# Performance work log

Measured on AMD Instinct MI355X. Metric: run time of the kernel, lower is better.

## Reference

```python
import jax, jax.numpy as jnp
import numpy as np
import math

D_MODEL = 1024
HEADS = 16
HEAD_DIM = D_MODEL // HEADS
BATCH = 2
SEQ = 2048


def setup_inputs() -> dict:
    key = jax.random.key(0)
    ks = jax.random.split(key, 6)
    scale = 1.0 / math.sqrt(D_MODEL)
    return {
        "x": jax.random.normal(ks[0], (BATCH, SEQ, D_MODEL), dtype=jnp.float32),
        "mask": jnp.zeros((SEQ, SEQ), dtype=jnp.float32),
        "w_qkv": jax.random.normal(ks[1], (D_MODEL, 3 * D_MODEL), dtype=jnp.float32) * scale,
        "b_qkv": jax.random.normal(ks[2], (3 * D_MODEL,), dtype=jnp.float32) * 0.01,
        "w_out": jax.random.normal(ks[3], (D_MODEL, D_MODEL), dtype=jnp.float32) * scale,
        "b_out": jax.random.normal(ks[4], (D_MODEL,), dtype=jnp.float32) * 0.01,
    }


def reference(x, mask, w_qkv, b_qkv, w_out, b_out):
    B, S, D = x.shape
    H, hd = HEADS, HEAD_DIM
    # fused QKV projection: [B,S,3D]
    qkv = x @ w_qkv + b_qkv
    # [B,S,H,3*hd] -> [B,H,S,3*hd]
    qkv = qkv.reshape(B, S, H, 3 * hd).transpose(0, 2, 1, 3)
    q, k, v = jnp.split(qkv, 3, axis=-1)  # each [B,H,S,hd]
    inv_sqrt_d = jnp.asarray(1.0 / math.sqrt(hd), dtype=x.dtype)
    scores = jnp.einsum("bhqd,bhkd->bhqk", q, k) * inv_sqrt_d
    # additive mask; [S,S] broadcasts identically in [H,B,S,S] or [B,H,S,S] layout
    scores = scores + mask
    attn = jax.nn.softmax(scores, axis=-1)
    vals = jnp.einsum("bhqk,bhkd->bhqd", attn, v)  # [B,H,S,hd]
    vals = vals.transpose(0, 2, 1, 3).reshape(B, S, H * hd)
    return vals @ w_out + b_out
```

## Files before the change

kernel.cpp:

```cpp
#include <hip/hip_runtime.h>


typedef __bf16 bf16;
typedef __bf16 bf16x2 __attribute__((ext_vector_type(2)));
typedef __bf16 bf16x4 __attribute__((ext_vector_type(4)));
typedef __bf16 bf16x8 __attribute__((ext_vector_type(8)));
typedef float f32x4 __attribute__((ext_vector_type(4)));

#define MFMA(a, b, c) __builtin_amdgcn_mfma_f32_16x16x32_bf16((a), (b), (c), 0, 0, 0)

#if __has_builtin(__builtin_amdgcn_exp2f)
#define EXP2(x) __builtin_amdgcn_exp2f(x)
#else
#define EXP2(x) exp2f(x)
#endif

__device__ __forceinline__ void load_lds16(const bf16* g, void* l) {
    __builtin_amdgcn_global_load_lds(
        (const __attribute__((address_space(1))) unsigned int*)g,
        (__attribute__((address_space(3))) unsigned int*)l, 16, 0, 0);
}

__global__ void cast4_kernel(const float* __restrict__ in, bf16* __restrict__ out, int n4) {
    int i = blockIdx.x * blockDim.x + threadIdx.x;
    if (i < n4) {
        float4 v = ((const float4*)in)[i];
        bf16x4 o = {(bf16)v.x, (bf16)v.y, (bf16)v.z, (bf16)v.w};
        ((bf16x4*)out)[i] = o;
    }
}

__global__ void transpose_cast_kernel(const float* __restrict__ in, bf16* __restrict__ out,
                                      int R, int C) {
    __shared__ float tile[32][33];
    int bx = blockIdx.x * 32;
    int by = blockIdx.y * 32;
    int tx = threadIdx.x, ty = threadIdx.y;
    for (int i = 0; i < 32; i += 8)
        tile[ty + i][tx] = in[(size_t)(by + ty + i) * C + bx + tx];
    __syncthreads();
    for (int i = 0; i < 32; i += 8)
        out[(size_t)(bx + ty + i) * R + by + tx] = (bf16)tile[tx][ty + i];
}


#define GEMM_PROLOG(KDIM)                                                        \
    __shared__ __attribute__((aligned(16))) bf16 As[128 * 32];                   \
    __shared__ __attribute__((aligned(16))) bf16 Bs[128 * 32];                   \
    int bm = blockIdx.x, bn = blockIdx.y;                                        \
    int t = threadIdx.x;                                                         \
    int w = t >> 6, lane = t & 63, g = lane >> 4, l16 = lane & 15;               \
    int wm = (w >> 1) * 64, wn = (w & 1) * 64;                                   \
    f32x4 acc[4][4] = {};                                                        \
    const bf16* Ablk = A + (size_t)(bm * 128) * KDIM;                            \
    const bf16* Bblk = BT + (size_t)(bn * 128) * KDIM;                           \
    int srow = t >> 2;                                                           \
    int scg = (t & 3) ^ (srow & 3);       \
    const bf16* ag0 = Ablk + (size_t)srow * KDIM + scg * 8;                      \
    const bf16* ag1 = Ablk + (size_t)(srow + 64) * KDIM + scg * 8;               \
    const bf16* bg0 = Bblk + (size_t)srow * KDIM + scg * 8;                      \
    const bf16* bg1 = Bblk + (size_t)(srow + 64) * KDIM + scg * 8;               \
    char* asl = (char*)As;                                                       \
    char* bsl = (char*)Bs;                                                       \
    for (int kb = 0; kb < KDIM; kb += 32) {                                      \
        __syncthreads();                                                         \
        load_lds16(ag0 + kb, asl + t * 16);                                      \
        load_lds16(ag1 + kb, asl + 4096 + t * 16);                               \
        load_lds16(bg0 + kb, bsl + t * 16);                                      \
        load_lds16(bg1 + kb, bsl + 4096 + t * 16);                               \
        __syncthreads();                                                         \
        bf16x8 af[4], bfr[4];                                                    \
        int sw = l16 & 3;                                                        \
        for (int mi = 0; mi < 4; mi++) {                                         \
            int row = wm + mi * 16 + l16;                                        \
            af[mi] = *(const bf16x8*)(&As[row * 32 + (g ^ sw) * 8]);             \
        }                                                                        \
        for (int ni = 0; ni < 4; ni++) {                                         \
            int row = wn + ni * 16 + l16;                                        \
            bfr[ni] = *(const bf16x8*)(&Bs[row * 32 + (g ^ sw) * 8]);            \
        }                                                                        \
        for (int mi = 0; mi < 4; mi++)                                           \
            for (int ni = 0; ni < 4; ni++)                                       \
                acc[mi][ni] = MFMA(af[mi], bfr[ni], acc[mi][ni]);                \
    }

__global__ __launch_bounds__(256) void gemm_qkv_kernel(
    const bf16* __restrict__ A, const bf16* __restrict__ BT,
    const float* __restrict__ bias,
    bf16* __restrict__ Q, bf16* __restrict__ K, bf16* __restrict__ VT) {
    GEMM_PROLOG(1024)

    for (int mi = 0; mi < 4; mi++) {
        int row0 = bm * 128 + wm + mi * 16 + g * 4;
        int b = row0 >> 11, s0 = row0 & 2047;
        for (int ni = 0; ni < 4; ni++) {
            int col = bn * 128 + wn + ni * 16 + l16;
            float bv = bias[col];
            int h = col / 192, tt = col % 192;
            size_t bh = (size_t)(b * 16 + h);
            if (tt < 128) {
                bf16* dst = (tt < 64) ? &Q[(bh * 2048 + s0) * 64 + tt]
                                      : &K[(bh * 2048 + s0) * 64 + (tt - 64)];
                for (int r = 0; r < 4; r++)
                    dst[(size_t)r * 64] = (bf16)(acc[mi][ni][r] + bv);
            } else {
                bf16x4 pk = {(bf16)(acc[mi][ni][0] + bv), (bf16)(acc[mi][ni][1] + bv),
                             (bf16)(acc[mi][ni][2] + bv), (bf16)(acc[mi][ni][3] + bv)};
                *(bf16x4*)(&VT[(bh * 64 + (tt - 128)) * 2048 + s0]) = pk;
            }
        }
    }
}

__global__ __launch_bounds__(256) void gemm_out_kernel(
    const bf16* __restrict__ A, const bf16* __restrict__ BT,
    const float* __restrict__ bias, float* __restrict__ out) {
    GEMM_PROLOG(1024)

    for (int mi = 0; mi < 4; mi++) {
        for (int ni = 0; ni < 4; ni++) {
            int col = bn * 128 + wn + ni * 16 + l16;
            float bv = bias[col];
            for (int r = 0; r < 4; r++) {
                int row = bm * 128 + wm + mi * 16 + g * 4 + r;
                out[(size_t)row * 1024 + col] = acc[mi][ni][r] + bv;
            }
        }
    }
}

__global__ __launch_bounds__(256, 4) void attn_kernel(
    const bf16* __restrict__ Q, const bf16* __restrict__ K,
    const bf16* __restrict__ VT, const float* __restrict__ mask,
    bf16* __restrict__ vals) {
    __shared__ __attribute__((aligned(16))) char lds[4][8192];

    int blk = blockIdx.x;
    int bh = ((blk & 7) << 2) | ((blk >> 3) & 3);
    int qt = blk >> 5;
    int t = threadIdx.x;
    int w = t >> 6, lane = t & 63, g = lane >> 4, l16 = lane & 15;
    int qw = qt * 64 + w * 16;

    const bf16* Qp = Q + (size_t)bh * 2048 * 64;
    const bf16* Kp = K + (size_t)bh * 2048 * 64;
    const bf16* Vp = VT + (size_t)bh * 64 * 2048;
    const float* mrow = mask + (size_t)(qw + l16) * 2048;

    int ks_row = t >> 3;
    int ks_cblk = (t & 7) ^ (ks_row & 7);
    const bf16* kg = Kp + ks_row * 64 + ks_cblk * 8;
    int vs_d = t >> 2;
    int vs_sblk = (t & 3) ^ ((t >> 3) & 3);
    const bf16* vg = Vp + (size_t)vs_d * 2048 + vs_sblk * 8;

    const float SCL = 0.125f * 1.44269504089f;
    const float L2E = 1.44269504089f;

    bf16x8 q0 = *(const bf16x8*)(&Qp[(size_t)(qw + l16) * 64 + g * 8]);
    bf16x8 q1 = *(const bf16x8*)(&Qp[(size_t)(qw + l16) * 64 + 32 + g * 8]);
    load_lds16(kg + 0, &lds[0][t * 16]);
    load_lds16(vg + 0, &lds[0][4096 + t * 16]);
    float4 mv0 = *(const float4*)(&mrow[0 + g * 4]);
    float4 mv1 = *(const float4*)(&mrow[16 + g * 4]);
    load_lds16(kg + 1 * 32 * 64, &lds[1][t * 16]);
    load_lds16(vg + 1 * 32, &lds[1][4096 + t * 16]);
    asm volatile("s_waitcnt vmcnt(0)" ::: "memory");
    asm volatile("s_barrier" ::: "memory");

    f32x4 o[4] = {};
    float m = -1e30f, l = 0.f;

    for (int j = 0; j < 64; j++) {
        int buf = j & 3;
        int jm = j + 1 < 64 ? j + 1 : 63;
        float4 nmv0 = *(const float4*)(&mrow[jm * 32 + g * 4]);
        float4 nmv1 = *(const float4*)(&mrow[jm * 32 + 16 + g * 4]);
        int jp = j + 2 < 64 ? j + 2 : 63;
        load_lds16(kg + (size_t)jp * 32 * 64, &lds[(j + 2) & 3][t * 16]);
        load_lds16(vg + jp * 32, &lds[(j + 2) & 3][4096 + t * 16]);
        asm volatile("s_waitcnt vmcnt(8)" ::: "memory");
        asm volatile("s_barrier" ::: "memory");

        float sc[8];
#pragma unroll
        for (int ts = 0; ts < 2; ts++) {
            int s0 = ts * 16 + l16;
            int sw = s0 & 7;
            bf16x8 k0 = *(const bf16x8*)(&lds[buf][(s0 * 8 + (g ^ sw)) * 16]);
            bf16x8 k1 = *(const bf16x8*)(&lds[buf][(s0 * 8 + ((4 + g) ^ sw)) * 16]);
            f32x4 st = {};
            st = MFMA(k0, q0, st);
            st = MFMA(k1, q1, st);
            float4 mv = ts ? *(float4*)&mv1 : *(float4*)&mv0;
            sc[ts * 4 + 0] = st[0] * SCL + mv.x * L2E;
            sc[ts * 4 + 1] = st[1] * SCL + mv.y * L2E;
            sc[ts * 4 + 2] = st[2] * SCL + mv.z * L2E;
            sc[ts * 4 + 3] = st[3] * SCL + mv.w * L2E;
        }

        float vmax = sc[0];
#pragma unroll
        for (int i = 1; i < 8; i++) vmax = fmaxf(vmax, sc[i]);
        vmax = fmaxf(vmax, __shfl_xor(vmax, 16, 64));
        vmax = fmaxf(vmax, __shfl_xor(vmax, 32, 64));
        float mn = fmaxf(m, vmax);
        float alpha = EXP2(m - mn);
        m = mn;
        float p[8], rs = 0.f;
#pragma unroll
        for (int i = 0; i < 8; i++) { p[i] = EXP2(sc[i] - mn); rs += p[i]; }
        rs += __shfl_xor(rs, 16, 64);
        rs += __shfl_xor(rs, 32, 64);
        l = l * alpha + rs;
#pragma unroll
        for (int nc = 0; nc < 4; nc++) {
            o[nc][0] *= alpha; o[nc][1] *= alpha; o[nc][2] *= alpha; o[nc][3] *= alpha;
        }

        int dw0, dw1, dw2, dw3;
        { union { bf16x2 h; int i; } u;
          u.h = bf16x2{(bf16)p[0], (bf16)p[1]}; dw0 = u.i;
          u.h = bf16x2{(bf16)p[2], (bf16)p[3]}; dw1 = u.i;
          u.h = bf16x2{(bf16)p[4], (bf16)p[5]}; dw2 = u.i;
          u.h = bf16x2{(bf16)p[6], (bf16)p[7]}; dw3 = u.i; }
        int selA = (((2 * g) & 3) << 4) | l16;
        int selB = (((2 * g + 1) & 3) << 4) | l16;
        int t0a = __shfl(dw0, selA, 64), t2a = __shfl(dw2, selA, 64);
        int t1a = __shfl(dw1, selA, 64), t3a = __shfl(dw3, selA, 64);
        int t0b = __shfl(dw0, selB, 64), t2b = __shfl(dw2, selB, 64);
        int t1b = __shfl(dw1, selB, 64), t3b = __shfl(dw3, selB, 64);
        bool hi = (g & 2) != 0;
        union { int i[4]; bf16x8 v; } pu;
        pu.i[0] = hi ? t2a : t0a;
        pu.i[1] = hi ? t3a : t1a;
        pu.i[2] = hi ? t2b : t0b;
        pu.i[3] = hi ? t3b : t1b;

#pragma unroll
        for (int nc = 0; nc < 4; nc++) {
            int d = nc * 16 + l16;
            int slot = d * 4 + (g ^ ((d >> 1) & 3));
            bf16x8 vf = *(const bf16x8*)(&lds[buf][4096 + slot * 16]);
            o[nc] = MFMA(vf, pu.v, o[nc]);
        }

        mv0 = nmv0;
        mv1 = nmv1;
    }

    int b = bh >> 4, h = bh & 15;
    float linv = 1.f / l;
    size_t row = (size_t)(b * 2048 + qw + l16);
#pragma unroll
    for (int nc = 0; nc < 4; nc++) {
        bf16x4 pk = {(bf16)(o[nc][0] * linv), (bf16)(o[nc][1] * linv),
                     (bf16)(o[nc][2] * linv), (bf16)(o[nc][3] * linv)};
        *(bf16x4*)(&vals[row * 1024 + h * 64 + nc * 16 + g * 4]) = pk;
    }
}

extern "C" void kernel_launch(void* const* d_in, const int* in_sizes, int n_in,
                              void* d_out, int out_size, void* d_ws, size_t ws_size,
                              hipStream_t stream) {
    const float* x     = (const float*)d_in[0];
    const float* mask  = (const float*)d_in[1];
    const float* w_qkv = (const float*)d_in[2];
    const float* b_qkv = (const float*)d_in[3];
    const float* w_out = (const float*)d_in[4];
    const float* b_out = (const float*)d_in[5];
    float* out = (float*)d_out;

    char* ws = (char*)d_ws;
    size_t off = 0;
    bf16* xb    = (bf16*)(ws + off); off += (size_t)4096 * 1024 * 2;
    bf16* wqkvT = (bf16*)(ws + off); off += (size_t)3072 * 1024 * 2;
    bf16* woutT = (bf16*)(ws + off); off += (size_t)1024 * 1024 * 2;
    bf16* Qa    = (bf16*)(ws + off); off += (size_t)32 * 2048 * 64 * 2;
    bf16* Ka    = (bf16*)(ws + off); off += (size_t)32 * 2048 * 64 * 2;
    bf16* VTa   = (bf16*)(ws + off); off += (size_t)32 * 64 * 2048 * 2;
    bf16* vals  = (bf16*)(ws + off); off += (size_t)4096 * 1024 * 2;

    cast4_kernel<<<4096, 256, 0, stream>>>(x, xb, 4096 * 1024 / 4);
    transpose_cast_kernel<<<dim3(96, 32), dim3(32, 8), 0, stream>>>(w_qkv, wqkvT, 1024, 3072);
    transpose_cast_kernel<<<dim3(32, 32), dim3(32, 8), 0, stream>>>(w_out, woutT, 1024, 1024);
    gemm_qkv_kernel<<<dim3(32, 24), 256, 0, stream>>>(xb, wqkvT, b_qkv, Qa, Ka, VTa);
    attn_kernel<<<1024, 256, 0, stream>>>(Qa, Ka, VTa, mask, vals);
    gemm_out_kernel<<<dim3(32, 8), 256, 0, stream>>>(vals, woutT, b_out, out);
}
```

Measured before the change: 248.7 us.

## Pipeline GEMM loads through 4-stage LDS ring, shrink out-GEMM tile, skip softmax rescale

Both GEMMs now prefetch K-tiles two iterations ahead into a four-buffer LDS ring. Explicit vmcnt waits and raw barriers replace the double __syncthreads, so global-to-LDS loads overlap MFMA work. The output GEMM uses 128x64 tiles to double its grid and fill more CUs. The attention loop skips the alpha rescale of the accumulator when no lane's max increased, and the loops are unrolled. This costs more LDS per block and adds hand-written waitcnt logic that must match the issued load counts.

```diff
diff --git a/kernel.cpp b/kernel.cpp
--- a/kernel.cpp
+++ b/kernel.cpp
@@ -43,52 +43,69 @@
         out[(size_t)(bx + ty + i) * R + by + tx] = (bf16)tile[tx][ty + i];
 }
 
-
-#define GEMM_PROLOG(KDIM)                                                        \
-    __shared__ __attribute__((aligned(16))) bf16 As[128 * 32];                   \
-    __shared__ __attribute__((aligned(16))) bf16 Bs[128 * 32];                   \
-    int bm = blockIdx.x, bn = blockIdx.y;                                        \
-    int t = threadIdx.x;                                                         \
-    int w = t >> 6, lane = t & 63, g = lane >> 4, l16 = lane & 15;               \
-    int wm = (w >> 1) * 64, wn = (w & 1) * 64;                                   \
-    f32x4 acc[4][4] = {};                                                        \
-    const bf16* Ablk = A + (size_t)(bm * 128) * KDIM;                            \
-    const bf16* Bblk = BT + (size_t)(bn * 128) * KDIM;                           \
-    int srow = t >> 2;                                                           \
-    int scg = (t & 3) ^ (srow & 3);       \
-    const bf16* ag0 = Ablk + (size_t)srow * KDIM + scg * 8;                      \
-    const bf16* ag1 = Ablk + (size_t)(srow + 64) * KDIM + scg * 8;               \
-    const bf16* bg0 = Bblk + (size_t)srow * KDIM + scg * 8;                      \
-    const bf16* bg1 = Bblk + (size_t)(srow + 64) * KDIM + scg * 8;               \
-    char* asl = (char*)As;                                                       \
-    char* bsl = (char*)Bs;                                                       \
-    for (int kb = 0; kb < KDIM; kb += 32) {                                      \
-        __syncthreads();                                                         \
-        load_lds16(ag0 + kb, asl + t * 16);                                      \
-        load_lds16(ag1 + kb, asl + 4096 + t * 16);                               \
-        load_lds16(bg0 + kb, bsl + t * 16);                                      \
-        load_lds16(bg1 + kb, bsl + 4096 + t * 16);                               \
-        __syncthreads();                                                         \
-        bf16x8 af[4], bfr[4];                                                    \
-        int sw = l16 & 3;                                                        \
-        for (int mi = 0; mi < 4; mi++) {                                         \
-            int row = wm + mi * 16 + l16;                                        \
-            af[mi] = *(const bf16x8*)(&As[row * 32 + (g ^ sw) * 8]);             \
-        }                                                                        \
-        for (int ni = 0; ni < 4; ni++) {                                         \
-            int row = wn + ni * 16 + l16;                                        \
-            bfr[ni] = *(const bf16x8*)(&Bs[row * 32 + (g ^ sw) * 8]);            \
-        }                                                                        \
-        for (int mi = 0; mi < 4; mi++)                                           \
-            for (int ni = 0; ni < 4; ni++)                                       \
-                acc[mi][ni] = MFMA(af[mi], bfr[ni], acc[mi][ni]);                \
-    }
-
 __global__ __launch_bounds__(256) void gemm_qkv_kernel(
     const bf16* __restrict__ A, const bf16* __restrict__ BT,
     const float* __restrict__ bias,
     bf16* __restrict__ Q, bf16* __restrict__ K, bf16* __restrict__ VT) {
-    GEMM_PROLOG(1024)
+    __shared__ __attribute__((aligned(16))) char lds[4][16384];
+    int bm = blockIdx.x, bn = blockIdx.y;
+    int t = threadIdx.x;
+    int w = t >> 6, lane = t & 63, g = lane >> 4, l16 = lane & 15;
+    int wm = (w >> 1) * 64, wn = (w & 1) * 64;
+    f32x4 acc[4][4] = {};
+    const bf16* Ablk = A + (size_t)(bm * 128) * 1024;
+    const bf16* Bblk = BT + (size_t)(bn * 128) * 1024;
+    int srow = t >> 2;
+    int scg = (t & 3) ^ (srow & 3);
+    const bf16* ag0 = Ablk + (size_t)srow * 1024 + scg * 8;
+    const bf16* ag1 = ag0 + 64 * 1024;
+    const bf16* bg0 = Bblk + (size_t)srow * 1024 + scg * 8;
+    const bf16* bg1 = bg0 + 64 * 1024;
+
+    load_lds16(ag0, lds[0] + t * 16);
+    load_lds16(ag1, lds[0] + 4096 + t * 16);
+    load_lds16(bg0, lds[0] + 8192 + t * 16);
+    load_lds16(bg1, lds[0] + 12288 + t * 16);
+    load_lds16(ag0 + 32, lds[1] + t * 16);
+    load_lds16(ag1 + 32, lds[1] + 4096 + t * 16);
+    load_lds16(bg0 + 32, lds[1] + 8192 + t * 16);
+    load_lds16(bg1 + 32, lds[1] + 12288 + t * 16);
+    asm volatile("s_waitcnt vmcnt(0)" ::: "memory");
+    asm volatile("s_barrier" ::: "memory");
+
+    int sw = l16 & 3;
+#pragma unroll 4
+    for (int j = 0; j < 32; j++) {
+        int buf = j & 3;
+        int jp = j + 2 < 32 ? j + 2 : 31;
+        char* dst = lds[(j + 2) & 3];
+        load_lds16(ag0 + jp * 32, dst + t * 16);
+        load_lds16(ag1 + jp * 32, dst + 4096 + t * 16);
+        load_lds16(bg0 + jp * 32, dst + 8192 + t * 16);
+        load_lds16(bg1 + jp * 32, dst + 12288 + t * 16);
+        asm volatile("s_waitcnt vmcnt(8)" ::: "memory");
+        asm volatile("s_barrier" ::: "memory");
+
+        const bf16* As = (const bf16*)lds[buf];
+        const bf16* Bs = (const bf16*)(lds[buf] + 8192);
+        bf16x8 af[4], bfr[4];
+#pragma unroll
+        for (int mi = 0; mi < 4; mi++) {
+            int row = wm + mi * 16 + l16;
+            af[mi] = *(const bf16x8*)(&As[row * 32 + (g ^ sw) * 8]);
+        }
+#pragma unroll
+        for (int ni = 0; ni < 4; ni++) {
+            int row = wn + ni * 16 + l16;
+            bfr[ni] = *(const bf16x8*)(&Bs[row * 32 + (g ^ sw) * 8]);
+        }
+#pragma unroll
+        for (int mi = 0; mi < 4; mi++)
+#pragma unroll
+            for (int ni = 0; ni < 4; ni++)
+                acc[mi][ni] = MFMA(af[mi], bfr[ni], acc[mi][ni]);
+    }
+    asm volatile("s_waitcnt vmcnt(0)" ::: "memory");
 
     for (int mi = 0; mi < 4; mi++) {
         int row0 = bm * 128 + wm + mi * 16 + g * 4;
@@ -115,11 +132,65 @@
 __global__ __launch_bounds__(256) void gemm_out_kernel(
     const bf16* __restrict__ A, const bf16* __restrict__ BT,
     const float* __restrict__ bias, float* __restrict__ out) {
-    GEMM_PROLOG(1024)
+    __shared__ __attribute__((aligned(16))) char lds[4][12288];
+    int bm = blockIdx.x, bn = blockIdx.y;
+    int t = threadIdx.x;
+    int w = t >> 6, lane = t & 63, g = lane >> 4, l16 = lane & 15;
+    int wm = (w >> 1) * 64, wn = (w & 1) * 32;
+    f32x4 acc[4][2] = {};
+    const bf16* Ablk = A + (size_t)(bm * 128) * 1024;
+    const bf16* Bblk = BT + (size_t)(bn * 64) * 1024;
+    int srow = t >> 2;
+    int scg = (t & 3) ^ (srow & 3);
+    const bf16* ag0 = Ablk + (size_t)srow * 1024 + scg * 8;
+    const bf16* ag1 = ag0 + 64 * 1024;
+    const bf16* bg0 = Bblk + (size_t)srow * 1024 + scg * 8;
+
+    load_lds16(ag0, lds[0] + t * 16);
+    load_lds16(ag1, lds[0] + 4096 + t * 16);
+    load_lds16(bg0, lds[0] + 8192 + t * 16);
+    load_lds16(ag0 + 32, lds[1] + t * 16);
+    load_lds16(ag1 + 32, lds[1] + 4096 + t * 16);
+    load_lds16(bg0 + 32, lds[1] + 8192 + t * 16);
+    asm volatile("s_waitcnt vmcnt(0)" ::: "memory");
+    asm volatile("s_barrier" ::: "memory");
+
+    int sw = l16 & 3;
+#pragma unroll 4
+    for (int j = 0; j < 32; j++) {
+        int buf = j & 3;
+        int jp = j + 2 < 32 ? j + 2 : 31;
+        char* dst = lds[(j + 2) & 3];
+        load_lds16(ag0 + jp * 32, dst + t * 16);
+        load_lds16(ag1 + jp * 32, dst + 4096 + t * 16);
+        load_lds16(bg0 + jp * 32, dst + 8192 + t * 16);
+        asm volatile("s_waitcnt vmcnt(6)" ::: "memory");
+        asm volatile("s_barrier" ::: "memory");
+
+        const bf16* As = (const bf16*)lds[buf];
+        const bf16* Bs = (const bf16*)(lds[buf] + 8192);
+        bf16x8 af[4], bfr[2];
+#pragma unroll
+        for (int mi = 0; mi < 4; mi++) {
+            int row = wm + mi * 16 + l16;
+            af[mi] = *(const bf16x8*)(&As[row * 32 + (g ^ sw) * 8]);
+        }
+#pragma unroll
+        for (int ni = 0; ni < 2; ni++) {
+            int row = wn + ni * 16 + l16;
+            bfr[ni] = *(const bf16x8*)(&Bs[row * 32 + (g ^ sw) * 8]);
+        }
+#pragma unroll
+        for (int mi = 0; mi < 4; mi++)
+#pragma unroll
+            for (int ni = 0; ni < 2; ni++)
+                acc[mi][ni] = MFMA(af[mi], bfr[ni], acc[mi][ni]);
+    }
+    asm volatile("s_waitcnt vmcnt(0)" ::: "memory");
 
     for (int mi = 0; mi < 4; mi++) {
-        for (int ni = 0; ni < 4; ni++) {
-            int col = bn * 128 + wn + ni * 16 + l16;
+        for (int ni = 0; ni < 2; ni++) {
+            int col = bn * 64 + wn + ni * 16 + l16;
             float bv = bias[col];
             for (int r = 0; r < 4; r++) {
                 int row = bm * 128 + wm + mi * 16 + g * 4 + r;
@@ -171,6 +242,7 @@
     f32x4 o[4] = {};
     float m = -1e30f, l = 0.f;
 
+#pragma unroll 4
     for (int j = 0; j < 64; j++) {
         int buf = j & 3;
         int jm = j + 1 < 64 ? j + 1 : 63;
@@ -204,18 +276,24 @@
         for (int i = 1; i < 8; i++) vmax = fmaxf(vmax, sc[i]);
         vmax = fmaxf(vmax, __shfl_xor(vmax, 16, 64));
         vmax = fmaxf(vmax, __shfl_xor(vmax, 32, 64));
-        float mn = fmaxf(m, vmax);
-        float alpha = EXP2(m - mn);
+        float mold = m;
+        float mn = fmaxf(mold, vmax);
         m = mn;
         float p[8], rs = 0.f;
 #pragma unroll
         for (int i = 0; i < 8; i++) { p[i] = EXP2(sc[i] - mn); rs += p[i]; }
         rs += __shfl_xor(rs, 16, 64);
         rs += __shfl_xor(rs, 32, 64);
-        l = l * alpha + rs;
-#pragma unroll
-        for (int nc = 0; nc < 4; nc++) {
-            o[nc][0] *= alpha; o[nc][1] *= alpha; o[nc][2] *= alpha; o[nc][3] *= alpha;
+        if (__any(vmax > mold)) {
+            float alpha = EXP2(mold - mn);
+            l = l * alpha + rs;
+#pragma unroll
+            for (int nc = 0; nc < 4; nc++) {
+                o[nc][0] *= alpha; o[nc][1] *= alpha;
+                o[nc][2] *= alpha; o[nc][3] *= alpha;
+            }
+        } else {
+            l += rs;
         }
 
         int dw0, dw1, dw2, dw3;
@@ -248,6 +326,7 @@
         mv0 = nmv0;
         mv1 = nmv1;
     }
+    asm volatile("s_waitcnt vmcnt(0)" ::: "memory");
 
     int b = bh >> 4, h = bh & 15;
     float linv = 1.f / l;
@@ -286,5 +365,5 @@
     transpose_cast_kernel<<<dim3(32, 32), dim3(32, 8), 0, stream>>>(w_out, woutT, 1024, 1024);
     gemm_qkv_kernel<<<dim3(32, 24), 256, 0, stream>>>(xb, wqkvT, b_qkv, Qa, Ka, VTa);
     attn_kernel<<<1024, 256, 0, stream>>>(Qa, Ka, VTa, mask, vals);
-    gemm_out_kernel<<<dim3(32, 8), 256, 0, stream>>>(vals, woutT, b_out, out);
-}
+    gemm_out_kernel<<<dim3(32, 16), 256, 0, stream>>>(vals, woutT, b_out, out);
+}
```

Result: faster. 240.9 us (-3.2%).
